# Performance work log

Measured on AMD Instinct MI355X. Metric: run time of the kernel, lower is better.

Reference implementation:

```python
import jax, jax.numpy as jnp
import numpy as np

N_NODES = 100000
N_EDGES = 3200000
EMBED_DIM = 64
BATCH = 16384


def setup_inputs() -> dict:
    key = jax.random.key(0)
    k1, k2, k3, k4 = jax.random.split(key, 4)
    gcn_weight = jax.random.normal(k1, (N_NODES, EMBED_DIM), dtype=jnp.float32) * 0.1
    gcn_bias = jnp.zeros((EMBED_DIM,), dtype=jnp.float32)
    linear_weight = jax.random.normal(k2, (N_NODES, 1), dtype=jnp.float32) * 0.1
    linear_bias = jnp.zeros((1,), dtype=jnp.float32)
    edge_index = jax.random.randint(k3, (2, N_EDGES), 0, N_NODES, dtype=jnp.int64)
    interaction_pairs = jax.random.randint(k4, (BATCH, 2), 0, N_NODES, dtype=jnp.int64)
    return {
        "gcn_weight": gcn_weight,
        "gcn_bias": gcn_bias,
        "linear_weight": linear_weight,
        "linear_bias": linear_bias,
        "edge_index": edge_index,
        "interaction_pairs": interaction_pairs,
    }


def _gcn_conv_identity_features(gcn_weight, gcn_bias, edge_index):
    # Features X = I, so X @ W = W. GCNConv output = D^{-1/2}(A+I)D^{-1/2} W + b.
    src, dst = edge_index[0], edge_index[1]
    ones = jnp.ones((src.shape[0],), dtype=gcn_weight.dtype)
    # degree (with self loop) computed on destination nodes, as in PyG gcn_norm
    deg = jax.ops.segment_sum(ones, dst, num_segments=N_NODES) + 1.0
    dinv = jax.lax.rsqrt(deg)  # [N]
    norm = dinv[src] * dinv[dst]  # [E]
    msg = gcn_weight[src] * norm[:, None]  # [E, D] -- dominant memory traffic
    agg = jax.ops.segment_sum(msg, dst, num_segments=N_NODES)  # [N, D]
    # self-loop term: norm_ii = 1/deg[i]
    out = agg + gcn_weight * (dinv * dinv)[:, None] + gcn_bias
    return out


def reference(gcn_weight, gcn_bias, linear_weight, linear_bias, edge_index, interaction_pairs):
    node_emb = _gcn_conv_identity_features(gcn_weight, gcn_bias, edge_index)  # [N, D]
    e = node_emb[interaction_pairs]  # [B, 2, D] gather
    # FM pairwise interaction: 0.5 * sum_d ((sum_f e)^2 - sum_f e^2)
    sum_sq = jnp.square(jnp.sum(e, axis=1))  # [B, D]
    sq_sum = jnp.sum(jnp.square(e), axis=1)  # [B, D]
    fm = 0.5 * jnp.sum(sum_sq - sq_sum, axis=1, keepdims=True)  # [B, 1]
    # FeaturesLinear: sum of per-node scalar embeddings + bias
    lin = jnp.sum(linear_weight[interaction_pairs], axis=1) + linear_bias  # [B, 1]
    return jnp.squeeze(lin + fm, axis=1)  # [B]
```

## Files before the change

kernel.cpp:

```cpp
#include <hip/hip_runtime.h>

#define N_NODES 100000
#define N_EDGES 3200000
#define BATCH 16384
#define MAX_SLOTS 32768

#define NW 12500
#define SLICES 256
#define EPS2 12500
#define I4PS2 3125

#define CAP 128

#define OFF_SLOT      0
#define OFF_DINV      400064
#define OFF_NODELIST  800064
#define OFF_SCOUNT    931136
#define OFF_PARTIALS  1062208
#define OFF_WH        13862208
#define OFF_BINS2     26662208
#define OFF_EMB       43439424

__device__ __forceinline__ unsigned bfr(float f) {
    unsigned u = __float_as_uint(f);
    return (u + 0x7FFFu + ((u >> 16) & 1u)) >> 16;
}
__device__ __forceinline__ float bfx(unsigned h) {
    return __uint_as_float(h << 16);
}

__global__ void k_flags(const int* __restrict__ pairs, unsigned* __restrict__ slot,
                        int* __restrict__ nodelist, int* __restrict__ scount) {
    int i = blockIdx.x * blockDim.x + threadIdx.x;
    if (i < 2 * BATCH) {
        int n = pairs[i];
        nodelist[i] = n;
        slot[n] = (unsigned)(i + 1);
        scount[i] = 0;
    }
}

__device__ __forceinline__ int cert(int d, const unsigned* __restrict__ slot,
                                    const int* __restrict__ nodelist) {
    unsigned r = slot[d];
    unsigned idx = r - 1u;
    if (idx < (unsigned)MAX_SLOTS && nodelist[idx] == d) return (int)idx;
    return -1;
}

__global__ void k_fused(const int* __restrict__ src, const int* __restrict__ dst,
                        const unsigned* __restrict__ slot, const int* __restrict__ nodelist,
                        unsigned* __restrict__ partials,
                        int* __restrict__ scount, int* __restrict__ bins2) {
    __shared__ unsigned h[NW];
    int g = blockIdx.x;
    for (int i = threadIdx.x; i < NW; i += 1024) h[i] = 0;
    __syncthreads();
    const int4* d4 = (const int4*)(dst + g * EPS2);
    const int4* s4 = (const int4*)(src + g * EPS2);
    for (int i = threadIdx.x; i < I4PS2; i += 1024) {
        int4 v = d4[i];
        int4 s = s4[i];
        atomicAdd(&h[v.x >> 3], 1u << ((v.x & 7) << 2));
        atomicAdd(&h[v.y >> 3], 1u << ((v.y & 7) << 2));
        atomicAdd(&h[v.z >> 3], 1u << ((v.z & 7) << 2));
        atomicAdd(&h[v.w >> 3], 1u << ((v.w & 7) << 2));
        int t;
        t = cert(v.x, slot, nodelist);
        if (t >= 0) { int p = atomicAdd(&scount[t], 1); if (p < CAP) bins2[(t << 7) + p] = s.x; }
        t = cert(v.y, slot, nodelist);
        if (t >= 0) { int p = atomicAdd(&scount[t], 1); if (p < CAP) bins2[(t << 7) + p] = s.y; }
        t = cert(v.z, slot, nodelist);
        if (t >= 0) { int p = atomicAdd(&scount[t], 1); if (p < CAP) bins2[(t << 7) + p] = s.z; }
        t = cert(v.w, slot, nodelist);
        if (t >= 0) { int p = atomicAdd(&scount[t], 1); if (p < CAP) bins2[(t << 7) + p] = s.w; }
    }
    __syncthreads();
    unsigned* outp = partials + (unsigned)g * NW;
    for (int i = threadIdx.x; i < NW; i += 1024) outp[i] = h[i];
}

__global__ void k_mid(const unsigned* __restrict__ partials, const float4* __restrict__ w4,
                      float* __restrict__ dinv, uint4* __restrict__ wh4) {
    __shared__ unsigned pA[256], pB[256], pC[256], pD[256];
    __shared__ float sdinv[256];
    int blk = blockIdx.x;
    int wi = threadIdx.x & 31, sg = threadIdx.x >> 5;
    int w = blk * 32 + wi;
    unsigned A = 0, B = 0, C = 0, D = 0;
    if (w < NW) {
        const unsigned* q = partials + w;
#pragma unroll
        for (int ch = 0; ch < 2; ++ch) {
            unsigned x = 0, y = 0;
#pragma unroll
            for (int k = 0; k < 16; ++k) {
                unsigned v = q[(unsigned)(sg * 32 + ch * 16 + k) * NW];
                x += v & 0x0F0F0F0Fu;
                y += (v >> 4) & 0x0F0F0F0Fu;
            }
            A += x & 0x00FF00FFu;
            B += (x >> 8) & 0x00FF00FFu;
            C += y & 0x00FF00FFu;
            D += (y >> 8) & 0x00FF00FFu;
        }
    }
    pA[threadIdx.x] = A; pB[threadIdx.x] = B; pC[threadIdx.x] = C; pD[threadIdx.x] = D;
    __syncthreads();
    if (threadIdx.x < 32 && w < NW) {
        unsigned sA = 0, sB = 0, sC = 0, sD = 0;
#pragma unroll
        for (int k = 0; k < 8; ++k) {
            sA += pA[k * 32 + wi]; sB += pB[k * 32 + wi];
            sC += pC[k * 32 + wi]; sD += pD[k * 32 + wi];
        }
        float4 d0, d1;
        d0.x = rsqrtf((float)(sA & 0xFFFFu) + 1.0f);
        d0.y = rsqrtf((float)(sC & 0xFFFFu) + 1.0f);
        d0.z = rsqrtf((float)(sB & 0xFFFFu) + 1.0f);
        d0.w = rsqrtf((float)(sD & 0xFFFFu) + 1.0f);
        d1.x = rsqrtf((float)(sA >> 16) + 1.0f);
        d1.y = rsqrtf((float)(sC >> 16) + 1.0f);
        d1.z = rsqrtf((float)(sB >> 16) + 1.0f);
        d1.w = rsqrtf((float)(sD >> 16) + 1.0f);
        ((float4*)dinv)[w * 2] = d0;
        ((float4*)dinv)[w * 2 + 1] = d1;
        int lb = wi * 8;
        sdinv[lb + 0] = d0.x; sdinv[lb + 1] = d0.y; sdinv[lb + 2] = d0.z; sdinv[lb + 3] = d0.w;
        sdinv[lb + 4] = d1.x; sdinv[lb + 5] = d1.y; sdinv[lb + 6] = d1.z; sdinv[lb + 7] = d1.w;
    }
    __syncthreads();
#pragma unroll
    for (int it = 0; it < 8; ++it) {
        int k = blk * 2048 + it * 256 + threadIdx.x;
        if (k < N_NODES * 8) {
            float4 va = w4[k * 2];
            float4 vb = w4[k * 2 + 1];
            float d = sdinv[(k >> 3) - blk * 256];
            uint4 o;
            o.x = bfr(va.x * d) | (bfr(va.y * d) << 16);
            o.y = bfr(va.z * d) | (bfr(va.w * d) << 16);
            o.z = bfr(vb.x * d) | (bfr(vb.y * d) << 16);
            o.w = bfr(vb.z * d) | (bfr(vb.w * d) << 16);
            wh4[k] = o;
        }
    }
}

__global__ void k_gather(const int* __restrict__ nodelist, const int* __restrict__ scount,
                         const int* __restrict__ bins2, const uint4* __restrict__ wh4,
                         const float* __restrict__ dinv, const float4* __restrict__ bias4,
                         uint4* __restrict__ emb4) {
    int s = (blockIdx.x * blockDim.x + threadIdx.x) >> 6;
    int lane = threadIdx.x & 63;
    int rg = lane >> 3, dp = lane & 7;
    int cnt = scount[s];
    const int* bp = bins2 + (s << 7);
    double a0 = 0., a1 = 0., a2 = 0., a3 = 0., a4 = 0., a5 = 0., a6 = 0., a7 = 0.;
    int j = 0;
    for (; j + 16 <= cnt; j += 16) {
        int e0 = bp[j + rg];
        int e1 = bp[j + 8 + rg];
        uint4 oa = wh4[(e0 << 3) + dp];
        uint4 ob = wh4[(e1 << 3) + dp];
        a0 += (double)(bfx(oa.x) + bfx(ob.x));
        a1 += (double)(bfx(oa.x >> 16) + bfx(ob.x >> 16));
        a2 += (double)(bfx(oa.y) + bfx(ob.y));
        a3 += (double)(bfx(oa.y >> 16) + bfx(ob.y >> 16));
        a4 += (double)(bfx(oa.z) + bfx(ob.z));
        a5 += (double)(bfx(oa.z >> 16) + bfx(ob.z >> 16));
        a6 += (double)(bfx(oa.w) + bfx(ob.w));
        a7 += (double)(bfx(oa.w >> 16) + bfx(ob.w >> 16));
    }
    for (; j < cnt; j += 8) {
        if (rg < cnt - j) {
            int e0 = bp[j + rg];
            uint4 oa = wh4[(e0 << 3) + dp];
            a0 += (double)bfx(oa.x); a1 += (double)bfx(oa.x >> 16);
            a2 += (double)bfx(oa.y); a3 += (double)bfx(oa.y >> 16);
            a4 += (double)bfx(oa.z); a5 += (double)bfx(oa.z >> 16);
            a6 += (double)bfx(oa.w); a7 += (double)bfx(oa.w >> 16);
        }
    }
#pragma unroll
    for (int m = 8; m <= 32; m <<= 1) {
        a0 += __shfl_xor(a0, m, 64); a1 += __shfl_xor(a1, m, 64);
        a2 += __shfl_xor(a2, m, 64); a3 += __shfl_xor(a3, m, 64);
        a4 += __shfl_xor(a4, m, 64); a5 += __shfl_xor(a5, m, 64);
        a6 += __shfl_xor(a6, m, 64); a7 += __shfl_xor(a7, m, 64);
    }
    if (rg == 0) {
        int n = nodelist[s];
        float dn = dinv[n];
        uint4 u = wh4[(n << 3) + dp];
        float4 b0 = bias4[dp * 2], b1 = bias4[dp * 2 + 1];
        float r0 = ((float)a0 + bfx(u.x)) * dn + b0.x;
        float r1 = ((float)a1 + bfx(u.x >> 16)) * dn + b0.y;
        float r2 = ((float)a2 + bfx(u.y)) * dn + b0.z;
        float r3 = ((float)a3 + bfx(u.y >> 16)) * dn + b0.w;
        float r4 = ((float)a4 + bfx(u.z)) * dn + b1.x;
        float r5 = ((float)a5 + bfx(u.z >> 16)) * dn + b1.y;
        float r6 = ((float)a6 + bfx(u.w)) * dn + b1.z;
        float r7 = ((float)a7 + bfx(u.w >> 16)) * dn + b1.w;
        uint4 o;
        o.x = bfr(r0) | (bfr(r1) << 16);
        o.y = bfr(r2) | (bfr(r3) << 16);
        o.z = bfr(r4) | (bfr(r5) << 16);
        o.w = bfr(r6) | (bfr(r7) << 16);
        emb4[(s << 3) + dp] = o;
    }
}

__global__ void k_final(const int* __restrict__ pairs, const unsigned* __restrict__ slot,
                        const uint2* __restrict__ emb2, const float* __restrict__ lw,
                        const float* __restrict__ lb, float* __restrict__ out) {
    int p = (blockIdx.x * blockDim.x + threadIdx.x) >> 4;
    int li = threadIdx.x & 15;
    if (p >= BATCH) return;
    int a = pairs[p * 2], b = pairs[p * 2 + 1];
    int sa = (int)slot[a] - 1;
    int sb = (int)slot[b] - 1;
    uint2 ua = emb2[(sa << 4) + li];
    uint2 ub = emb2[(sb << 4) + li];
    float prod = bfx(ua.x) * bfx(ub.x) + bfx(ua.x >> 16) * bfx(ub.x >> 16)
               + bfx(ua.y) * bfx(ub.y) + bfx(ua.y >> 16) * bfx(ub.y >> 16);
#pragma unroll
    for (int m = 1; m <= 8; m <<= 1) prod += __shfl_xor(prod, m, 64);
    if (li == 0) out[p] = lw[a] + lw[b] + lb[0] + prod;
}

extern "C" void kernel_launch(void* const* d_in, const int* in_sizes, int n_in,
                              void* d_out, int out_size, void* d_ws, size_t ws_size,
                              hipStream_t stream) {
    const float* gcn_weight    = (const float*)d_in[0];
    const float* gcn_bias      = (const float*)d_in[1];
    const float* linear_weight = (const float*)d_in[2];
    const float* linear_bias   = (const float*)d_in[3];
    const int*   edge_index    = (const int*)d_in[4];
    const int*   pairs         = (const int*)d_in[5];
    float* out = (float*)d_out;

    char* ws = (char*)d_ws;
    unsigned* slot      = (unsigned*)(ws + OFF_SLOT);
    float*    dinv      = (float*)   (ws + OFF_DINV);
    int*      nodelist  = (int*)     (ws + OFF_NODELIST);
    int*      scount    = (int*)     (ws + OFF_SCOUNT);
    unsigned* partials  = (unsigned*)(ws + OFF_PARTIALS);
    uint4*    wh4       = (uint4*)   (ws + OFF_WH);
    int*      bins2     = (int*)     (ws + OFF_BINS2);
    uint4*    emb4      = (uint4*)   (ws + OFF_EMB);
    uint2*    emb2      = (uint2*)   (ws + OFF_EMB);

    const int* src_arr = edge_index;
    const int* dst_arr = edge_index + N_EDGES;

    k_flags<<<128, 256, 0, stream>>>(pairs, slot, nodelist, scount);
    k_fused<<<SLICES, 1024, 0, stream>>>(src_arr, dst_arr, slot, nodelist,
                                         partials, scount, bins2);
    k_mid<<<391, 256, 0, stream>>>(partials, (const float4*)gcn_weight, dinv, wh4);
    k_gather<<<MAX_SLOTS / 4, 256, 0, stream>>>(nodelist, scount, bins2, wh4,
                                                dinv, (const float4*)gcn_bias, emb4);
    k_final<<<1024, 256, 0, stream>>>(pairs, slot, emb2, linear_weight, linear_bias, out);
}
```

Before: 192.0 us.

## Replace slot-certification lookups with shared-memory bitmap and node-indexed bins

```diff
diff --git a/kernel.cpp b/kernel.cpp
--- a/kernel.cpp
+++ b/kernel.cpp
@@ -6,6 +6,7 @@
 #define MAX_SLOTS 32768
 
 #define NW 12500
+#define BMW 3125
 #define SLICES 256
 #define EPS2 12500
 #define I4PS2 3125
@@ -13,13 +14,16 @@
 #define CAP 128
 
 #define OFF_SLOT      0
-#define OFF_DINV      400064
-#define OFF_NODELIST  800064
-#define OFF_SCOUNT    931136
-#define OFF_PARTIALS  1062208
-#define OFF_WH        13862208
-#define OFF_BINS2     26662208
-#define OFF_EMB       43439424
+#define OFF_DINV      400000
+#define OFF_NODELIST  800000
+#define OFF_BITMAP    931072
+#define OFF_NCOUNT    943600
+#define OFF_PARTIALS  1343600
+#define OFF_WH        14143600
+#define OFF_BINS2     26943600
+#define OFF_EMB       78143600
+
+#define ZERO_WORDS 103132
 
 __device__ __forceinline__ unsigned bfr(float f) {
     unsigned u = __float_as_uint(f);
@@ -29,32 +33,31 @@
     return __uint_as_float(h << 16);
 }
 
+__global__ void k_zero(unsigned* __restrict__ base) {
+    int i = blockIdx.x * blockDim.x + threadIdx.x;
+    for (; i < ZERO_WORDS; i += gridDim.x * blockDim.x) base[i] = 0;
+}
+
 __global__ void k_flags(const int* __restrict__ pairs, unsigned* __restrict__ slot,
-                        int* __restrict__ nodelist, int* __restrict__ scount) {
+                        int* __restrict__ nodelist, unsigned* __restrict__ bitmap) {
     int i = blockIdx.x * blockDim.x + threadIdx.x;
     if (i < 2 * BATCH) {
         int n = pairs[i];
         nodelist[i] = n;
         slot[n] = (unsigned)(i + 1);
-        scount[i] = 0;
-    }
-}
-
-__device__ __forceinline__ int cert(int d, const unsigned* __restrict__ slot,
-                                    const int* __restrict__ nodelist) {
-    unsigned r = slot[d];
-    unsigned idx = r - 1u;
-    if (idx < (unsigned)MAX_SLOTS && nodelist[idx] == d) return (int)idx;
-    return -1;
+        atomicOr(&bitmap[n >> 5], 1u << (n & 31));
+    }
 }
 
 __global__ void k_fused(const int* __restrict__ src, const int* __restrict__ dst,
-                        const unsigned* __restrict__ slot, const int* __restrict__ nodelist,
+                        const unsigned* __restrict__ bitmap,
                         unsigned* __restrict__ partials,
-                        int* __restrict__ scount, int* __restrict__ bins2) {
+                        int* __restrict__ ncount, int* __restrict__ bins2) {
     __shared__ unsigned h[NW];
+    __shared__ unsigned bm[BMW];
     int g = blockIdx.x;
     for (int i = threadIdx.x; i < NW; i += 1024) h[i] = 0;
+    for (int i = threadIdx.x; i < BMW; i += 1024) bm[i] = bitmap[i];
     __syncthreads();
     const int4* d4 = (const int4*)(dst + g * EPS2);
     const int4* s4 = (const int4*)(src + g * EPS2);
@@ -65,15 +68,22 @@
         atomicAdd(&h[v.y >> 3], 1u << ((v.y & 7) << 2));
         atomicAdd(&h[v.z >> 3], 1u << ((v.z & 7) << 2));
         atomicAdd(&h[v.w >> 3], 1u << ((v.w & 7) << 2));
-        int t;
-        t = cert(v.x, slot, nodelist);
-        if (t >= 0) { int p = atomicAdd(&scount[t], 1); if (p < CAP) bins2[(t << 7) + p] = s.x; }
-        t = cert(v.y, slot, nodelist);
-        if (t >= 0) { int p = atomicAdd(&scount[t], 1); if (p < CAP) bins2[(t << 7) + p] = s.y; }
-        t = cert(v.z, slot, nodelist);
-        if (t >= 0) { int p = atomicAdd(&scount[t], 1); if (p < CAP) bins2[(t << 7) + p] = s.z; }
-        t = cert(v.w, slot, nodelist);
-        if (t >= 0) { int p = atomicAdd(&scount[t], 1); if (p < CAP) bins2[(t << 7) + p] = s.w; }
+        if ((bm[v.x >> 5] >> (v.x & 31)) & 1u) {
+            int p = atomicAdd(&ncount[v.x], 1);
+            if (p < CAP) bins2[(v.x << 7) + p] = s.x;
+        }
+        if ((bm[v.y >> 5] >> (v.y & 31)) & 1u) {
+            int p = atomicAdd(&ncount[v.y], 1);
+            if (p < CAP) bins2[(v.y << 7) + p] = s.y;
+        }
+        if ((bm[v.z >> 5] >> (v.z & 31)) & 1u) {
+            int p = atomicAdd(&ncount[v.z], 1);
+            if (p < CAP) bins2[(v.z << 7) + p] = s.z;
+        }
+        if ((bm[v.w >> 5] >> (v.w & 31)) & 1u) {
+            int p = atomicAdd(&ncount[v.w], 1);
+            if (p < CAP) bins2[(v.w << 7) + p] = s.w;
+        }
     }
     __syncthreads();
     unsigned* outp = partials + (unsigned)g * NW;
@@ -147,15 +157,16 @@
     }
 }
 
-__global__ void k_gather(const int* __restrict__ nodelist, const int* __restrict__ scount,
+__global__ void k_gather(const int* __restrict__ nodelist, const int* __restrict__ ncount,
                          const int* __restrict__ bins2, const uint4* __restrict__ wh4,
                          const float* __restrict__ dinv, const float4* __restrict__ bias4,
                          uint4* __restrict__ emb4) {
     int s = (blockIdx.x * blockDim.x + threadIdx.x) >> 6;
     int lane = threadIdx.x & 63;
     int rg = lane >> 3, dp = lane & 7;
-    int cnt = scount[s];
-    const int* bp = bins2 + (s << 7);
+    int n = nodelist[s];
+    int cnt = ncount[n];
+    const int* bp = bins2 + (n << 7);
     double a0 = 0., a1 = 0., a2 = 0., a3 = 0., a4 = 0., a5 = 0., a6 = 0., a7 = 0.;
     int j = 0;
     for (; j + 16 <= cnt; j += 16) {
@@ -190,7 +201,6 @@
         a6 += __shfl_xor(a6, m, 64); a7 += __shfl_xor(a7, m, 64);
     }
     if (rg == 0) {
-        int n = nodelist[s];
         float dn = dinv[n];
         uint4 u = wh4[(n << 3) + dp];
         float4 b0 = bias4[dp * 2], b1 = bias4[dp * 2 + 1];
@@ -244,7 +254,8 @@
     unsigned* slot      = (unsigned*)(ws + OFF_SLOT);
     float*    dinv      = (float*)   (ws + OFF_DINV);
     int*      nodelist  = (int*)     (ws + OFF_NODELIST);
-    int*      scount    = (int*)     (ws + OFF_SCOUNT);
+    unsigned* bitmap    = (unsigned*)(ws + OFF_BITMAP);
+    int*      ncount    = (int*)     (ws + OFF_NCOUNT);
     unsigned* partials  = (unsigned*)(ws + OFF_PARTIALS);
     uint4*    wh4       = (uint4*)   (ws + OFF_WH);
     int*      bins2     = (int*)     (ws + OFF_BINS2);
@@ -254,11 +265,11 @@
     const int* src_arr = edge_index;
     const int* dst_arr = edge_index + N_EDGES;
 
-    k_flags<<<128, 256, 0, stream>>>(pairs, slot, nodelist, scount);
-    k_fused<<<SLICES, 1024, 0, stream>>>(src_arr, dst_arr, slot, nodelist,
-                                         partials, scount, bins2);
+    k_zero<<<128, 1024, 0, stream>>>(bitmap);
+    k_flags<<<128, 256, 0, stream>>>(pairs, slot, nodelist, bitmap);
+    k_fused<<<SLICES, 1024, 0, stream>>>(src_arr, dst_arr, bitmap, partials, ncount, bins2);
     k_mid<<<391, 256, 0, stream>>>(partials, (const float4*)gcn_weight, dinv, wh4);
-    k_gather<<<MAX_SLOTS / 4, 256, 0, stream>>>(nodelist, scount, bins2, wh4,
+    k_gather<<<MAX_SLOTS / 4, 256, 0, stream>>>(nodelist, ncount, bins2, wh4,
                                                 dinv, (const float4*)gcn_bias, emb4);
     k_final<<<1024, 256, 0, stream>>>(pairs, slot, emb2, linear_weight, linear_bias, out);
 }
```

Measured after the change: 198.7 us. +3.5%, slower.

## Replace per-block shared-memory degree histograms with global atomic degree counts

Applied to the files above, without the earlier changes.

```diff
diff --git a/kernel.cpp b/kernel.cpp
--- a/kernel.cpp
+++ b/kernel.cpp
@@ -5,21 +5,16 @@
 #define BATCH 16384
 #define MAX_SLOTS 32768
 
-#define NW 12500
-#define SLICES 256
-#define EPS2 12500
-#define I4PS2 3125
-
 #define CAP 128
 
 #define OFF_SLOT      0
-#define OFF_DINV      400064
-#define OFF_NODELIST  800064
-#define OFF_SCOUNT    931136
-#define OFF_PARTIALS  1062208
-#define OFF_WH        13862208
-#define OFF_BINS2     26662208
-#define OFF_EMB       43439424
+#define OFF_DEG       400000
+#define OFF_DINV      800000
+#define OFF_NODELIST  1200000
+#define OFF_SCOUNT    1331072
+#define OFF_WH        1462144
+#define OFF_BINS2     14262144
+#define OFF_EMB       31039360
 
 __device__ __forceinline__ unsigned bfr(float f) {
     unsigned u = __float_as_uint(f);
@@ -30,8 +25,10 @@
 }
 
 __global__ void k_flags(const int* __restrict__ pairs, unsigned* __restrict__ slot,
-                        int* __restrict__ nodelist, int* __restrict__ scount) {
+                        int* __restrict__ nodelist, unsigned* __restrict__ deg,
+                        int* __restrict__ scount) {
     int i = blockIdx.x * blockDim.x + threadIdx.x;
+    if (i < N_NODES) deg[i] = 0;
     if (i < 2 * BATCH) {
         int n = pairs[i];
         nodelist[i] = n;
@@ -48,103 +45,47 @@
     return -1;
 }
 
-__global__ void k_fused(const int* __restrict__ src, const int* __restrict__ dst,
-                        const unsigned* __restrict__ slot, const int* __restrict__ nodelist,
-                        unsigned* __restrict__ partials,
-                        int* __restrict__ scount, int* __restrict__ bins2) {
-    __shared__ unsigned h[NW];
-    int g = blockIdx.x;
-    for (int i = threadIdx.x; i < NW; i += 1024) h[i] = 0;
-    __syncthreads();
-    const int4* d4 = (const int4*)(dst + g * EPS2);
-    const int4* s4 = (const int4*)(src + g * EPS2);
-    for (int i = threadIdx.x; i < I4PS2; i += 1024) {
-        int4 v = d4[i];
-        int4 s = s4[i];
-        atomicAdd(&h[v.x >> 3], 1u << ((v.x & 7) << 2));
-        atomicAdd(&h[v.y >> 3], 1u << ((v.y & 7) << 2));
-        atomicAdd(&h[v.z >> 3], 1u << ((v.z & 7) << 2));
-        atomicAdd(&h[v.w >> 3], 1u << ((v.w & 7) << 2));
+__global__ void k_edge(const int4* __restrict__ src4, const int4* __restrict__ dst4,
+                       const unsigned* __restrict__ slot, const int* __restrict__ nodelist,
+                       unsigned* __restrict__ deg, int* __restrict__ scount,
+                       int* __restrict__ bins2) {
+    const int NI4 = N_EDGES / 4;
+    int i = blockIdx.x * blockDim.x + threadIdx.x;
+    int stride = gridDim.x * blockDim.x;
+    for (; i < NI4; i += stride) {
+        int4 d = dst4[i];
+        int4 s = src4[i];
+        atomicAdd(&deg[d.x], 1u);
+        atomicAdd(&deg[d.y], 1u);
+        atomicAdd(&deg[d.z], 1u);
+        atomicAdd(&deg[d.w], 1u);
         int t;
-        t = cert(v.x, slot, nodelist);
+        t = cert(d.x, slot, nodelist);
         if (t >= 0) { int p = atomicAdd(&scount[t], 1); if (p < CAP) bins2[(t << 7) + p] = s.x; }
-        t = cert(v.y, slot, nodelist);
+        t = cert(d.y, slot, nodelist);
         if (t >= 0) { int p = atomicAdd(&scount[t], 1); if (p < CAP) bins2[(t << 7) + p] = s.y; }
-        t = cert(v.z, slot, nodelist);
+        t = cert(d.z, slot, nodelist);
         if (t >= 0) { int p = atomicAdd(&scount[t], 1); if (p < CAP) bins2[(t << 7) + p] = s.z; }
-        t = cert(v.w, slot, nodelist);
+        t = cert(d.w, slot, nodelist);
         if (t >= 0) { int p = atomicAdd(&scount[t], 1); if (p < CAP) bins2[(t << 7) + p] = s.w; }
     }
-    __syncthreads();
-    unsigned* outp = partials + (unsigned)g * NW;
-    for (int i = threadIdx.x; i < NW; i += 1024) outp[i] = h[i];
-}
-
-__global__ void k_mid(const unsigned* __restrict__ partials, const float4* __restrict__ w4,
+}
+
+__global__ void k_mid(const unsigned* __restrict__ deg, const float4* __restrict__ w4,
                       float* __restrict__ dinv, uint4* __restrict__ wh4) {
-    __shared__ unsigned pA[256], pB[256], pC[256], pD[256];
-    __shared__ float sdinv[256];
-    int blk = blockIdx.x;
-    int wi = threadIdx.x & 31, sg = threadIdx.x >> 5;
-    int w = blk * 32 + wi;
-    unsigned A = 0, B = 0, C = 0, D = 0;
-    if (w < NW) {
-        const unsigned* q = partials + w;
-#pragma unroll
-        for (int ch = 0; ch < 2; ++ch) {
-            unsigned x = 0, y = 0;
-#pragma unroll
-            for (int k = 0; k < 16; ++k) {
-                unsigned v = q[(unsigned)(sg * 32 + ch * 16 + k) * NW];
-                x += v & 0x0F0F0F0Fu;
-                y += (v >> 4) & 0x0F0F0F0Fu;
-            }
-            A += x & 0x00FF00FFu;
-            B += (x >> 8) & 0x00FF00FFu;
-            C += y & 0x00FF00FFu;
-            D += (y >> 8) & 0x00FF00FFu;
-        }
-    }
-    pA[threadIdx.x] = A; pB[threadIdx.x] = B; pC[threadIdx.x] = C; pD[threadIdx.x] = D;
-    __syncthreads();
-    if (threadIdx.x < 32 && w < NW) {
-        unsigned sA = 0, sB = 0, sC = 0, sD = 0;
-#pragma unroll
-        for (int k = 0; k < 8; ++k) {
-            sA += pA[k * 32 + wi]; sB += pB[k * 32 + wi];
-            sC += pC[k * 32 + wi]; sD += pD[k * 32 + wi];
-        }
-        float4 d0, d1;
-        d0.x = rsqrtf((float)(sA & 0xFFFFu) + 1.0f);
-        d0.y = rsqrtf((float)(sC & 0xFFFFu) + 1.0f);
-        d0.z = rsqrtf((float)(sB & 0xFFFFu) + 1.0f);
-        d0.w = rsqrtf((float)(sD & 0xFFFFu) + 1.0f);
-        d1.x = rsqrtf((float)(sA >> 16) + 1.0f);
-        d1.y = rsqrtf((float)(sC >> 16) + 1.0f);
-        d1.z = rsqrtf((float)(sB >> 16) + 1.0f);
-        d1.w = rsqrtf((float)(sD >> 16) + 1.0f);
-        ((float4*)dinv)[w * 2] = d0;
-        ((float4*)dinv)[w * 2 + 1] = d1;
-        int lb = wi * 8;
-        sdinv[lb + 0] = d0.x; sdinv[lb + 1] = d0.y; sdinv[lb + 2] = d0.z; sdinv[lb + 3] = d0.w;
-        sdinv[lb + 4] = d1.x; sdinv[lb + 5] = d1.y; sdinv[lb + 6] = d1.z; sdinv[lb + 7] = d1.w;
-    }
-    __syncthreads();
-#pragma unroll
-    for (int it = 0; it < 8; ++it) {
-        int k = blk * 2048 + it * 256 + threadIdx.x;
-        if (k < N_NODES * 8) {
-            float4 va = w4[k * 2];
-            float4 vb = w4[k * 2 + 1];
-            float d = sdinv[(k >> 3) - blk * 256];
-            uint4 o;
-            o.x = bfr(va.x * d) | (bfr(va.y * d) << 16);
-            o.y = bfr(va.z * d) | (bfr(va.w * d) << 16);
-            o.z = bfr(vb.x * d) | (bfr(vb.y * d) << 16);
-            o.w = bfr(vb.z * d) | (bfr(vb.w * d) << 16);
-            wh4[k] = o;
-        }
-    }
+    int k = blockIdx.x * blockDim.x + threadIdx.x;
+    if (k >= N_NODES * 8) return;
+    int n = k >> 3;
+    float d = rsqrtf((float)deg[n] + 1.0f);
+    float4 va = w4[k * 2];
+    float4 vb = w4[k * 2 + 1];
+    uint4 o;
+    o.x = bfr(va.x * d) | (bfr(va.y * d) << 16);
+    o.y = bfr(va.z * d) | (bfr(va.w * d) << 16);
+    o.z = bfr(vb.x * d) | (bfr(vb.y * d) << 16);
+    o.w = bfr(vb.z * d) | (bfr(vb.w * d) << 16);
+    wh4[k] = o;
+    if ((k & 7) == 0) dinv[n] = d;
 }
 
 __global__ void k_gather(const int* __restrict__ nodelist, const int* __restrict__ scount,
@@ -155,6 +96,7 @@
     int lane = threadIdx.x & 63;
     int rg = lane >> 3, dp = lane & 7;
     int cnt = scount[s];
+    if (cnt > CAP) cnt = CAP;
     const int* bp = bins2 + (s << 7);
     double a0 = 0., a1 = 0., a2 = 0., a3 = 0., a4 = 0., a5 = 0., a6 = 0., a7 = 0.;
     int j = 0;
@@ -242,10 +184,10 @@
 
     char* ws = (char*)d_ws;
     unsigned* slot      = (unsigned*)(ws + OFF_SLOT);
+    unsigned* deg       = (unsigned*)(ws + OFF_DEG);
     float*    dinv      = (float*)   (ws + OFF_DINV);
     int*      nodelist  = (int*)     (ws + OFF_NODELIST);
     int*      scount    = (int*)     (ws + OFF_SCOUNT);
-    unsigned* partials  = (unsigned*)(ws + OFF_PARTIALS);
     uint4*    wh4       = (uint4*)   (ws + OFF_WH);
     int*      bins2     = (int*)     (ws + OFF_BINS2);
     uint4*    emb4      = (uint4*)   (ws + OFF_EMB);
@@ -254,10 +196,11 @@
     const int* src_arr = edge_index;
     const int* dst_arr = edge_index + N_EDGES;
 
-    k_flags<<<128, 256, 0, stream>>>(pairs, slot, nodelist, scount);
-    k_fused<<<SLICES, 1024, 0, stream>>>(src_arr, dst_arr, slot, nodelist,
-                                         partials, scount, bins2);
-    k_mid<<<391, 256, 0, stream>>>(partials, (const float4*)gcn_weight, dinv, wh4);
+    k_flags<<<196, 512, 0, stream>>>(pairs, slot, nodelist, deg, scount);
+    k_edge<<<2048, 256, 0, stream>>>((const int4*)src_arr, (const int4*)dst_arr,
+                                     slot, nodelist, deg, scount, bins2);
+    k_mid<<<(N_NODES * 8 + 1023) / 1024, 1024, 0, stream>>>(deg, (const float4*)gcn_weight,
+                                                            dinv, wh4);
     k_gather<<<MAX_SLOTS / 4, 256, 0, stream>>>(nodelist, scount, bins2, wh4,
                                                 dinv, (const float4*)gcn_bias, emb4);
     k_final<<<1024, 256, 0, stream>>>(pairs, slot, emb2, linear_weight, linear_bias, out);
```

Result: slower. 296.9 us (+54.6%).

## Replace per-slot global atomic binning with two-level bucketed edge binning

Applied to the files above, without the earlier changes.

```diff
diff --git a/kernel.cpp b/kernel.cpp
--- a/kernel.cpp
+++ b/kernel.cpp
@@ -10,16 +10,19 @@
 #define EPS2 12500
 #define I4PS2 3125
 
-#define CAP 128
+#define NBUCK 256
+#define BCAP 8192
+#define BCAP_SH 13
+#define EBCAP 4608
 
 #define OFF_SLOT      0
-#define OFF_DINV      400064
-#define OFF_NODELIST  800064
-#define OFF_SCOUNT    931136
-#define OFF_PARTIALS  1062208
-#define OFF_WH        13862208
-#define OFF_BINS2     26662208
-#define OFF_EMB       43439424
+#define OFF_DINV      400000
+#define OFF_NODELIST  800000
+#define OFF_GCUR      931072
+#define OFF_PARTIALS  932096
+#define OFF_WH        13732096
+#define OFF_BINS      26532096
+#define OFF_EMB       34920704
 
 __device__ __forceinline__ unsigned bfr(float f) {
     unsigned u = __float_as_uint(f);
@@ -30,13 +33,13 @@
 }
 
 __global__ void k_flags(const int* __restrict__ pairs, unsigned* __restrict__ slot,
-                        int* __restrict__ nodelist, int* __restrict__ scount) {
+                        int* __restrict__ nodelist, unsigned* __restrict__ gcur) {
     int i = blockIdx.x * blockDim.x + threadIdx.x;
+    if (i < NBUCK) gcur[i] = (unsigned)(i << BCAP_SH);
     if (i < 2 * BATCH) {
         int n = pairs[i];
         nodelist[i] = n;
         slot[n] = (unsigned)(i + 1);
-        scount[i] = 0;
     }
 }
 
@@ -48,36 +51,69 @@
     return -1;
 }
 
-__global__ void k_fused(const int* __restrict__ src, const int* __restrict__ dst,
-                        const unsigned* __restrict__ slot, const int* __restrict__ nodelist,
-                        unsigned* __restrict__ partials,
-                        int* __restrict__ scount, int* __restrict__ bins2) {
+__global__ void k_hist(const int* __restrict__ src, const int* __restrict__ dst,
+                       const unsigned* __restrict__ slot, const int* __restrict__ nodelist,
+                       unsigned* __restrict__ partials, unsigned* __restrict__ gcur,
+                       unsigned* __restrict__ bins) {
     __shared__ unsigned h[NW];
+    __shared__ unsigned ebuf[EBCAP];
+    __shared__ int lc[NBUCK];
+    __shared__ int base[NBUCK];
+    __shared__ int ecnt;
     int g = blockIdx.x;
-    for (int i = threadIdx.x; i < NW; i += 1024) h[i] = 0;
+    int tid = threadIdx.x;
+    int lane = tid & 63;
+    for (int i = tid; i < NW; i += 512) h[i] = 0;
+    if (tid < NBUCK) lc[tid] = 0;
+    if (tid == 0) ecnt = 0;
     __syncthreads();
     const int4* d4 = (const int4*)(dst + g * EPS2);
     const int4* s4 = (const int4*)(src + g * EPS2);
-    for (int i = threadIdx.x; i < I4PS2; i += 1024) {
+    for (int i = tid; i < I4PS2; i += 512) {
         int4 v = d4[i];
         int4 s = s4[i];
         atomicAdd(&h[v.x >> 3], 1u << ((v.x & 7) << 2));
         atomicAdd(&h[v.y >> 3], 1u << ((v.y & 7) << 2));
         atomicAdd(&h[v.z >> 3], 1u << ((v.z & 7) << 2));
         atomicAdd(&h[v.w >> 3], 1u << ((v.w & 7) << 2));
-        int t;
-        t = cert(v.x, slot, nodelist);
-        if (t >= 0) { int p = atomicAdd(&scount[t], 1); if (p < CAP) bins2[(t << 7) + p] = s.x; }
-        t = cert(v.y, slot, nodelist);
-        if (t >= 0) { int p = atomicAdd(&scount[t], 1); if (p < CAP) bins2[(t << 7) + p] = s.y; }
-        t = cert(v.z, slot, nodelist);
-        if (t >= 0) { int p = atomicAdd(&scount[t], 1); if (p < CAP) bins2[(t << 7) + p] = s.z; }
-        t = cert(v.w, slot, nodelist);
-        if (t >= 0) { int p = atomicAdd(&scount[t], 1); if (p < CAP) bins2[(t << 7) + p] = s.w; }
+#define STAGE(dc, sc)                                                          \
+        {                                                                      \
+            int t = cert(dc, slot, nodelist);                                  \
+            unsigned long long mk = __ballot(t >= 0);                          \
+            int bs = 0;                                                        \
+            if (lane == 0) bs = atomicAdd(&ecnt, (int)__popcll(mk));           \
+            bs = __shfl(bs, 0, 64);                                            \
+            if (t >= 0) {                                                      \
+                int off = bs + (int)__popcll(mk & ((1ull << lane) - 1ull));    \
+                if (off < EBCAP) {                                             \
+                    ebuf[off] = ((unsigned)t << 17) | (unsigned)(sc);          \
+                    atomicAdd(&lc[t >> 7], 1);                                 \
+                }                                                              \
+            }                                                                  \
+        }
+        STAGE(v.x, s.x)
+        STAGE(v.y, s.y)
+        STAGE(v.z, s.z)
+        STAGE(v.w, s.w)
+#undef STAGE
     }
     __syncthreads();
     unsigned* outp = partials + (unsigned)g * NW;
-    for (int i = threadIdx.x; i < NW; i += 1024) outp[i] = h[i];
+    for (int i = tid; i < NW; i += 512) outp[i] = h[i];
+    if (tid < NBUCK) {
+        base[tid] = (int)atomicAdd(&gcur[tid], (unsigned)lc[tid]);
+        lc[tid] = 0;
+    }
+    __syncthreads();
+    int ne = ecnt;
+    if (ne > EBCAP) ne = EBCAP;
+    for (int j = tid; j < ne; j += 512) {
+        unsigned e = ebuf[j];
+        int b = (int)(e >> 24);
+        int r = atomicAdd(&lc[b], 1);
+        unsigned pos = (unsigned)base[b] + (unsigned)r;
+        if (pos < (unsigned)((b + 1) << BCAP_SH)) bins[pos] = e;
+    }
 }
 
 __global__ void k_mid(const unsigned* __restrict__ partials, const float4* __restrict__ w4,
@@ -147,67 +183,102 @@
     }
 }
 
-__global__ void k_gather(const int* __restrict__ nodelist, const int* __restrict__ scount,
-                         const int* __restrict__ bins2, const uint4* __restrict__ wh4,
-                         const float* __restrict__ dinv, const float4* __restrict__ bias4,
-                         uint4* __restrict__ emb4) {
-    int s = (blockIdx.x * blockDim.x + threadIdx.x) >> 6;
-    int lane = threadIdx.x & 63;
+__global__ void k_gfuse(const unsigned* __restrict__ gcur, const unsigned* __restrict__ bins,
+                        const int* __restrict__ nodelist, const uint4* __restrict__ wh4,
+                        const float* __restrict__ dinv, const float4* __restrict__ bias4,
+                        uint4* __restrict__ emb4) {
+    __shared__ unsigned ebuf2[BCAP];
+    __shared__ int lc[128], st[128];
+    int b = blockIdx.x >> 2;
+    int qt = blockIdx.x & 3;
+    int tid = threadIdx.x;
+    int cnt = (int)(gcur[b] - (unsigned)(b << BCAP_SH));
+    if (cnt > BCAP) cnt = BCAP;
+    const unsigned* bp = bins + ((unsigned)b << BCAP_SH);
+    if (tid < 128) lc[tid] = 0;
+    __syncthreads();
+    for (int j = tid; j < cnt; j += 512) atomicAdd(&lc[(bp[j] >> 17) & 127], 1);
+    __syncthreads();
+    if (tid < 128) st[tid] = lc[tid];
+    __syncthreads();
+    for (int off = 1; off < 128; off <<= 1) {
+        int v = (tid < 128 && tid >= off) ? st[tid - off] : 0;
+        __syncthreads();
+        if (tid < 128) st[tid] += v;
+        __syncthreads();
+    }
+    if (tid < 128) {
+        st[tid] -= lc[tid];
+        lc[tid] = st[tid];
+    }
+    __syncthreads();
+    for (int j = tid; j < cnt; j += 512) {
+        unsigned e = bp[j];
+        int r = atomicAdd(&lc[(e >> 17) & 127], 1);
+        ebuf2[r] = e & 0x1FFFFu;
+    }
+    __syncthreads();
+    int wave = tid >> 6, lane = tid & 63;
     int rg = lane >> 3, dp = lane & 7;
-    int cnt = scount[s];
-    const int* bp = bins2 + (s << 7);
-    double a0 = 0., a1 = 0., a2 = 0., a3 = 0., a4 = 0., a5 = 0., a6 = 0., a7 = 0.;
-    int j = 0;
-    for (; j + 16 <= cnt; j += 16) {
-        int e0 = bp[j + rg];
-        int e1 = bp[j + 8 + rg];
-        uint4 oa = wh4[(e0 << 3) + dp];
-        uint4 ob = wh4[(e1 << 3) + dp];
-        a0 += (double)(bfx(oa.x) + bfx(ob.x));
-        a1 += (double)(bfx(oa.x >> 16) + bfx(ob.x >> 16));
-        a2 += (double)(bfx(oa.y) + bfx(ob.y));
-        a3 += (double)(bfx(oa.y >> 16) + bfx(ob.y >> 16));
-        a4 += (double)(bfx(oa.z) + bfx(ob.z));
-        a5 += (double)(bfx(oa.z >> 16) + bfx(ob.z >> 16));
-        a6 += (double)(bfx(oa.w) + bfx(ob.w));
-        a7 += (double)(bfx(oa.w >> 16) + bfx(ob.w >> 16));
-    }
-    for (; j < cnt; j += 8) {
-        if (rg < cnt - j) {
-            int e0 = bp[j + rg];
+#pragma unroll
+    for (int q = 0; q < 4; ++q) {
+        int sl = qt * 32 + wave * 4 + q;
+        int s0 = st[sl];
+        int cn = lc[sl] - s0;
+        double a0 = 0., a1 = 0., a2 = 0., a3 = 0., a4 = 0., a5 = 0., a6 = 0., a7 = 0.;
+        int j = 0;
+        for (; j + 16 <= cn; j += 16) {
+            int e0 = (int)ebuf2[s0 + j + rg];
+            int e1 = (int)ebuf2[s0 + j + 8 + rg];
             uint4 oa = wh4[(e0 << 3) + dp];
-            a0 += (double)bfx(oa.x); a1 += (double)bfx(oa.x >> 16);
-            a2 += (double)bfx(oa.y); a3 += (double)bfx(oa.y >> 16);
-            a4 += (double)bfx(oa.z); a5 += (double)bfx(oa.z >> 16);
-            a6 += (double)bfx(oa.w); a7 += (double)bfx(oa.w >> 16);
-        }
-    }
-#pragma unroll
-    for (int m = 8; m <= 32; m <<= 1) {
-        a0 += __shfl_xor(a0, m, 64); a1 += __shfl_xor(a1, m, 64);
-        a2 += __shfl_xor(a2, m, 64); a3 += __shfl_xor(a3, m, 64);
-        a4 += __shfl_xor(a4, m, 64); a5 += __shfl_xor(a5, m, 64);
-        a6 += __shfl_xor(a6, m, 64); a7 += __shfl_xor(a7, m, 64);
-    }
-    if (rg == 0) {
-        int n = nodelist[s];
-        float dn = dinv[n];
-        uint4 u = wh4[(n << 3) + dp];
-        float4 b0 = bias4[dp * 2], b1 = bias4[dp * 2 + 1];
-        float r0 = ((float)a0 + bfx(u.x)) * dn + b0.x;
-        float r1 = ((float)a1 + bfx(u.x >> 16)) * dn + b0.y;
-        float r2 = ((float)a2 + bfx(u.y)) * dn + b0.z;
-        float r3 = ((float)a3 + bfx(u.y >> 16)) * dn + b0.w;
-        float r4 = ((float)a4 + bfx(u.z)) * dn + b1.x;
-        float r5 = ((float)a5 + bfx(u.z >> 16)) * dn + b1.y;
-        float r6 = ((float)a6 + bfx(u.w)) * dn + b1.z;
-        float r7 = ((float)a7 + bfx(u.w >> 16)) * dn + b1.w;
-        uint4 o;
-        o.x = bfr(r0) | (bfr(r1) << 16);
-        o.y = bfr(r2) | (bfr(r3) << 16);
-        o.z = bfr(r4) | (bfr(r5) << 16);
-        o.w = bfr(r6) | (bfr(r7) << 16);
-        emb4[(s << 3) + dp] = o;
+            uint4 ob = wh4[(e1 << 3) + dp];
+            a0 += (double)(bfx(oa.x) + bfx(ob.x));
+            a1 += (double)(bfx(oa.x >> 16) + bfx(ob.x >> 16));
+            a2 += (double)(bfx(oa.y) + bfx(ob.y));
+            a3 += (double)(bfx(oa.y >> 16) + bfx(ob.y >> 16));
+            a4 += (double)(bfx(oa.z) + bfx(ob.z));
+            a5 += (double)(bfx(oa.z >> 16) + bfx(ob.z >> 16));
+            a6 += (double)(bfx(oa.w) + bfx(ob.w));
+            a7 += (double)(bfx(oa.w >> 16) + bfx(ob.w >> 16));
+        }
+        for (; j < cn; j += 8) {
+            if (rg < cn - j) {
+                int e0 = (int)ebuf2[s0 + j + rg];
+                uint4 oa = wh4[(e0 << 3) + dp];
+                a0 += (double)bfx(oa.x); a1 += (double)bfx(oa.x >> 16);
+                a2 += (double)bfx(oa.y); a3 += (double)bfx(oa.y >> 16);
+                a4 += (double)bfx(oa.z); a5 += (double)bfx(oa.z >> 16);
+                a6 += (double)bfx(oa.w); a7 += (double)bfx(oa.w >> 16);
+            }
+        }
+#pragma unroll
+        for (int m = 8; m <= 32; m <<= 1) {
+            a0 += __shfl_xor(a0, m, 64); a1 += __shfl_xor(a1, m, 64);
+            a2 += __shfl_xor(a2, m, 64); a3 += __shfl_xor(a3, m, 64);
+            a4 += __shfl_xor(a4, m, 64); a5 += __shfl_xor(a5, m, 64);
+            a6 += __shfl_xor(a6, m, 64); a7 += __shfl_xor(a7, m, 64);
+        }
+        if (rg == 0) {
+            int gslot = (b << 7) + sl;
+            int n = nodelist[gslot];
+            float dn = dinv[n];
+            uint4 u = wh4[(n << 3) + dp];
+            float4 b0 = bias4[dp * 2], b1 = bias4[dp * 2 + 1];
+            float r0 = ((float)a0 + bfx(u.x)) * dn + b0.x;
+            float r1 = ((float)a1 + bfx(u.x >> 16)) * dn + b0.y;
+            float r2 = ((float)a2 + bfx(u.y)) * dn + b0.z;
+            float r3 = ((float)a3 + bfx(u.y >> 16)) * dn + b0.w;
+            float r4 = ((float)a4 + bfx(u.z)) * dn + b1.x;
+            float r5 = ((float)a5 + bfx(u.z >> 16)) * dn + b1.y;
+            float r6 = ((float)a6 + bfx(u.w)) * dn + b1.z;
+            float r7 = ((float)a7 + bfx(u.w >> 16)) * dn + b1.w;
+            uint4 o;
+            o.x = bfr(r0) | (bfr(r1) << 16);
+            o.y = bfr(r2) | (bfr(r3) << 16);
+            o.z = bfr(r4) | (bfr(r5) << 16);
+            o.w = bfr(r6) | (bfr(r7) << 16);
+            emb4[(gslot << 3) + dp] = o;
+        }
     }
 }
 
@@ -244,21 +315,21 @@
     unsigned* slot      = (unsigned*)(ws + OFF_SLOT);
     float*    dinv      = (float*)   (ws + OFF_DINV);
     int*      nodelist  = (int*)     (ws + OFF_NODELIST);
-    int*      scount    = (int*)     (ws + OFF_SCOUNT);
+    unsigned* gcur      = (unsigned*)(ws + OFF_GCUR);
     unsigned* partials  = (unsigned*)(ws + OFF_PARTIALS);
     uint4*    wh4       = (uint4*)   (ws + OFF_WH);
-    int*      bins2     = (int*)     (ws + OFF_BINS2);
+    unsigned* bins      = (unsigned*)(ws + OFF_BINS);
     uint4*    emb4      = (uint4*)   (ws + OFF_EMB);
     uint2*    emb2      = (uint2*)   (ws + OFF_EMB);
 
     const int* src_arr = edge_index;
     const int* dst_arr = edge_index + N_EDGES;
 
-    k_flags<<<128, 256, 0, stream>>>(pairs, slot, nodelist, scount);
-    k_fused<<<SLICES, 1024, 0, stream>>>(src_arr, dst_arr, slot, nodelist,
-                                         partials, scount, bins2);
+    k_flags<<<64, 512, 0, stream>>>(pairs, slot, nodelist, gcur);
+    k_hist<<<SLICES, 512, 0, stream>>>(src_arr, dst_arr, slot, nodelist,
+                                       partials, gcur, bins);
     k_mid<<<391, 256, 0, stream>>>(partials, (const float4*)gcn_weight, dinv, wh4);
-    k_gather<<<MAX_SLOTS / 4, 256, 0, stream>>>(nodelist, scount, bins2, wh4,
-                                                dinv, (const float4*)gcn_bias, emb4);
+    k_gfuse<<<NBUCK * 4, 512, 0, stream>>>(gcur, bins, nodelist, wh4,
+                                           dinv, (const float4*)gcn_bias, emb4);
     k_final<<<1024, 256, 0, stream>>>(pairs, slot, emb2, linear_weight, linear_bias, out);
 }
```

Result: faster. 163.1 us (-15.1%).
